# Kernel optimization log

Hardware: AMD Instinct MI355X
Metric: run time of the kernel (lower is better)

Reference implementation:

```python
import jax, jax.numpy as jnp
import numpy as np

B, M, D = 512, 96, 512
H = 8            # num_heads
DH = D // H      # head dim
NC = 3           # num_clusters
BETA = 5
MEM = 1024       # memory_size
EPS = 1e-8


def _l2norm(x, axis=-1):
    # torch F.cosine_similarity clamps each norm at eps=1e-8
    n = jnp.linalg.norm(x, axis=axis, keepdims=True)
    return x / jnp.maximum(n, EPS)


def _dynamic_clustering(sims):
    # sims: (B, M). Sort descending, split into NC equal groups,
    # per-group mean and (unbiased) std. (dynamic_clustering is not
    # defined in the source repo; this is the assumed implementation.)
    s = -jnp.sort(-sims, axis=1)               # descending
    g = s.reshape(B, NC, M // NC)
    means = g.mean(axis=-1)                    # (B, NC)
    stds = jnp.std(g, axis=-1, ddof=1)         # (B, NC)
    return means, stds


def setup_inputs() -> dict:
    key = jax.random.key(0)
    ks = jax.random.split(key, 6)
    vis_global = jax.random.normal(ks[0], (B, D), dtype=jnp.float32)
    text_features = jax.random.normal(ks[1], (B, M, D), dtype=jnp.float32)
    scale = 1.0 / np.sqrt(D)
    in_proj_w = jax.random.normal(ks[2], (3 * D, D), dtype=jnp.float32) * scale
    in_proj_b = jnp.zeros((3 * D,), dtype=jnp.float32)
    out_proj_w = jax.random.normal(ks[3], (D, D), dtype=jnp.float32) * scale
    out_proj_b = jnp.zeros((D,), dtype=jnp.float32)
    text_memory = jax.random.normal(ks[4], (MEM, D), dtype=jnp.float32)
    tau_p_log = jnp.log(jnp.asarray(0.1, dtype=jnp.float32))
    tau_n_log = jnp.log(jnp.asarray(0.05, dtype=jnp.float32))
    return dict(vis_global=vis_global, text_features=text_features,
                in_proj_w=in_proj_w, in_proj_b=in_proj_b,
                out_proj_w=out_proj_w, out_proj_b=out_proj_b,
                text_memory=text_memory, tau_p_log=tau_p_log, tau_n_log=tau_n_log)


def reference(vis_global, text_features, in_proj_w, in_proj_b,
              out_proj_w, out_proj_b, text_memory, tau_p_log, tau_n_log):
    # --- dynamic clustering over visual-text cosine sims ---
    sims = jnp.einsum('bd,bmd->bm', _l2norm(vis_global), _l2norm(text_features))
    means, stds = _dynamic_clustering(sims)
    cluster_scores = means / (stds + 1e-6)     # (B, NC)

    # --- MultiheadAttention: 1-token query, M-token key/value ---
    wq, wk, wv = in_proj_w[:D], in_proj_w[D:2 * D], in_proj_w[2 * D:]
    bq, bk, bv = in_proj_b[:D], in_proj_b[D:2 * D], in_proj_b[2 * D:]
    q = (vis_global @ wq.T + bq).reshape(B, H, DH)              # (B,H,DH)
    k = (text_features @ wk.T + bk).reshape(B, M, H, DH)        # (B,M,H,DH)
    v = (text_features @ wv.T + bv).reshape(B, M, H, DH)
    attn = jax.nn.softmax(jnp.einsum('bhd,bmhd->bhm', q, k) / np.sqrt(DH), axis=-1)
    ctx = jnp.einsum('bhm,bmhd->bhd', attn, v).reshape(B, D)
    corrected = ctx @ out_proj_w.T + out_proj_b                 # (B, D)

    tau_p = jnp.exp(tau_p_log)
    tau_n = jnp.exp(tau_n_log)
    pos_sim = jnp.sum(_l2norm(vis_global) * _l2norm(corrected), axis=-1)  # (B,)

    # memory-bank scatter (ptr starts at 0) + negatives, all detached
    corr_sg = jax.lax.stop_gradient(corrected)
    mem = text_memory.at[0:B].set(corr_sg)
    all_negs = jnp.concatenate([jnp.roll(corr_sg, 1, axis=0), mem], axis=0)  # (B+MEM, D)

    neg_sims = _l2norm(vis_global) @ _l2norm(all_negs).T        # (B, B+MEM)
    hard_negs, _ = jax.lax.top_k(neg_sims, BETA)                # (B, BETA)

    pos_term = jnp.exp(pos_sim / tau_p)
    neg_terms = jnp.exp(hard_negs / tau_n).sum(axis=1)
    loss = -jnp.mean(jnp.log(pos_term / (pos_term + neg_terms + 1e-8)))
    return loss, corrected, cluster_scores
```

## Files before the change

### kernel.cpp

```cpp
#include <hip/hip_runtime.h>
#include <math.h>

typedef unsigned short u16;
typedef unsigned int u32;
typedef __attribute__((ext_vector_type(8))) short short8;
typedef __attribute__((ext_vector_type(4))) float f32x4;

#define EPS 1e-8f

__device__ inline float bf2f(u16 u) {
    union { u32 i; float f; } v; v.i = ((u32)u) << 16; return v.f;
}
__device__ inline u16 f2bf(float f) {
    union { float f; u32 u; } v; v.f = f;
    u32 r = v.u + 0x7fffu + ((v.u >> 16) & 1u);
    return (u16)(r >> 16);
}
__device__ inline u32 pack2(float a, float b) {
    return (u32)f2bf(a) | ((u32)f2bf(b) << 16);
}
__device__ inline float wave_sum(float v) {
    for (int off = 32; off; off >>= 1) v += __shfl_xor(v, off, 64);
    return v;
}

__global__ __launch_bounds__(256) void prep(const float* __restrict__ vis,
                                            const float* __restrict__ ipw,
                                            const float* __restrict__ opw,
                                            float* __restrict__ vis_n,
                                            u16* __restrict__ vis_nb,
                                            u16* __restrict__ vis_b,
                                            u16* __restrict__ wqb,
                                            u16* __restrict__ wvb,
                                            u16* __restrict__ wob,
                                            float* __restrict__ loss0)
{
    int bid = blockIdx.x;
    if (bid >= 128) {
        int i = ((bid - 128) * 256 + threadIdx.x) * 4;
        const float* src; u16* dst; int j;
        if (i < 262144)      { j = i;          src = ipw + j;          dst = wqb + j; }
        else if (i < 524288) { j = i - 262144; src = ipw + 524288 + j; dst = wvb + j; }
        else                 { j = i - 524288; src = opw + j;          dst = wob + j; }
        float4 v = *(const float4*)src;
        uint2 pk; pk.x = pack2(v.x, v.y); pk.y = pack2(v.z, v.w);
        *(uint2*)dst = pk;
        return;
    }
    if (bid == 0 && threadIdx.x == 0) loss0[0] = 0.0f;
    int wave = threadIdx.x >> 6, lane = threadIdx.x & 63;
    int b = bid * 4 + wave;
    const float* row = vis + b * 512 + lane * 8;
    float4 x0 = *(const float4*)row;
    float4 x1 = *(const float4*)(row + 4);
    uint4 rk;
    rk.x = pack2(x0.x, x0.y); rk.y = pack2(x0.z, x0.w);
    rk.z = pack2(x1.x, x1.y); rk.w = pack2(x1.z, x1.w);
    *(uint4*)(vis_b + b*512 + lane*8) = rk;
    float ss = x0.x*x0.x + x0.y*x0.y + x0.z*x0.z + x0.w*x0.w
             + x1.x*x1.x + x1.y*x1.y + x1.z*x1.z + x1.w*x1.w;
    ss = wave_sum(ss);
    float inv = 1.0f / fmaxf(sqrtf(ss), EPS);
    float4 y0, y1;
    y0.x = x0.x*inv; y0.y = x0.y*inv; y0.z = x0.z*inv; y0.w = x0.w*inv;
    y1.x = x1.x*inv; y1.y = x1.y*inv; y1.z = x1.z*inv; y1.w = x1.w*inv;
    *(float4*)(vis_n + b*512 + lane*8)     = y0;
    *(float4*)(vis_n + b*512 + lane*8 + 4) = y1;
    uint4 pk;
    pk.x = pack2(y0.x, y0.y); pk.y = pack2(y0.z, y0.w);
    pk.z = pack2(y1.x, y1.y); pk.w = pack2(y1.z, y1.w);
    *(uint4*)(vis_nb + b*512 + lane*8) = pk;
}

__global__ __launch_bounds__(256) void gemm64(const u16* __restrict__ A, int lda,
                                              const u16* __restrict__ B,
                                              const float* __restrict__ bias,
                                              float* __restrict__ Cf, int ldc)
{
    __shared__ __align__(16) u16 As[64 * 64];
    __shared__ __align__(16) u16 Bs[64 * 64];
    const int t = threadIdx.x, lane = t & 63, w = t >> 6;
    const int m0 = blockIdx.x * 64, n0 = blockIdx.y * 64;
    const int wm = (w >> 1) * 32, wn = (w & 1) * 32;
    const int l16 = lane & 15, quad = lane >> 4;
    const int srow = t >> 3, scol = (t & 7) * 8;

    f32x4 acc[2][2];
    for (int i = 0; i < 2; i++)
        for (int j = 0; j < 2; j++)
            for (int e = 0; e < 4; e++) acc[i][j][e] = 0.f;

    for (int ko = 0; ko < 512; ko += 64) {
        __syncthreads();
        #pragma unroll
        for (int i = 0; i < 2; i++) {
            int row = i * 32 + srow;
            *(uint4*)&As[row * 64 + scol] = *(const uint4*)&A[(size_t)(m0 + row) * lda + ko + scol];
            *(uint4*)&Bs[row * 64 + scol] = *(const uint4*)&B[(size_t)(n0 + row) * 512 + ko + scol];
        }
        __syncthreads();
        #pragma unroll
        for (int ks = 0; ks < 2; ks++) {
            short8 af[2], bfr[2];
            #pragma unroll
            for (int i = 0; i < 2; i++)
                af[i] = *(const short8*)&As[(wm + i * 16 + l16) * 64 + ks * 32 + quad * 8];
            #pragma unroll
            for (int j = 0; j < 2; j++)
                bfr[j] = *(const short8*)&Bs[(wn + j * 16 + l16) * 64 + ks * 32 + quad * 8];
            #pragma unroll
            for (int i = 0; i < 2; i++)
                #pragma unroll
                for (int j = 0; j < 2; j++)
                    acc[i][j] = __builtin_amdgcn_mfma_f32_16x16x32_bf16(af[i], bfr[j], acc[i][j], 0, 0, 0);
        }
    }
    for (int i = 0; i < 2; i++) {
        int row = m0 + wm + i * 16 + quad * 4;
        for (int j = 0; j < 2; j++) {
            int col = n0 + wn + j * 16 + l16;
            float bv = bias ? bias[col] : 0.f;
            for (int r = 0; r < 4; r++)
                Cf[(size_t)(row + r) * ldc + col] = acc[i][j][r] + bv;
        }
    }
}

__global__ __launch_bounds__(256) void gemm_head(const u16* __restrict__ u_allb,
                                                 const u16* __restrict__ wvb,
                                                 const float* __restrict__ bv,
                                                 u16* __restrict__ ctxb)
{
    const int h = blockIdx.y;
    const u16* A = u_allb + h * 512;
    const u16* B = wvb + (size_t)h * 64 * 512;
    __shared__ __align__(16) u16 As[64 * 64];
    __shared__ __align__(16) u16 Bs[64 * 64];
    const int t = threadIdx.x, lane = t & 63, w = t >> 6;
    const int m0 = blockIdx.x * 64;
    const int wm = (w >> 1) * 32, wn = (w & 1) * 32;
    const int l16 = lane & 15, quad = lane >> 4;
    const int srow = t >> 3, scol = (t & 7) * 8;

    f32x4 acc[2][2];
    for (int i = 0; i < 2; i++)
        for (int j = 0; j < 2; j++)
            for (int e = 0; e < 4; e++) acc[i][j][e] = 0.f;

    for (int ko = 0; ko < 512; ko += 64) {
        __syncthreads();
        #pragma unroll
        for (int i = 0; i < 2; i++) {
            int row = i * 32 + srow;
            *(uint4*)&As[row * 64 + scol] = *(const uint4*)&A[(size_t)(m0 + row) * 4096 + ko + scol];
            *(uint4*)&Bs[row * 64 + scol] = *(const uint4*)&B[(size_t)row * 512 + ko + scol];
        }
        __syncthreads();
        #pragma unroll
        for (int ks = 0; ks < 2; ks++) {
            short8 af[2], bfr[2];
            #pragma unroll
            for (int i = 0; i < 2; i++)
                af[i] = *(const short8*)&As[(wm + i * 16 + l16) * 64 + ks * 32 + quad * 8];
            #pragma unroll
            for (int j = 0; j < 2; j++)
                bfr[j] = *(const short8*)&Bs[(wn + j * 16 + l16) * 64 + ks * 32 + quad * 8];
            #pragma unroll
            for (int i = 0; i < 2; i++)
                #pragma unroll
                for (int j = 0; j < 2; j++)
                    acc[i][j] = __builtin_amdgcn_mfma_f32_16x16x32_bf16(af[i], bfr[j], acc[i][j], 0, 0, 0);
        }
    }
    for (int i = 0; i < 2; i++) {
        int row = m0 + wm + i * 16 + quad * 4;
        for (int j = 0; j < 2; j++) {
            int col = wn + j * 16 + l16;
            float bb = bv[h * 64 + col];
            for (int r = 0; r < 4; r++)
                ctxb[(size_t)(row + r) * 512 + h * 64 + col] = f2bf(acc[i][j][r] + bb);
        }
    }
}

__global__ __launch_bounds__(256) void qk_proj(const float* __restrict__ q,
                                               const float* __restrict__ wk,
                                               float* __restrict__ qk_all)
{
    int bg = blockIdx.x, h = blockIdx.y;
    int t = threadIdx.x;
    int j = blockIdx.z * 256 + t;
    __shared__ float q8[8][64];
    {
        int r = t >> 5;
        int d0 = (t & 31) * 2;
        const float* qp = q + (bg * 8 + r) * 512 + h * 64 + d0;
        q8[r][d0] = qp[0]; q8[r][d0 + 1] = qp[1];
    }
    __syncthreads();
    float acc[8] = {0, 0, 0, 0, 0, 0, 0, 0};
    const float* wrow = wk + (size_t)(h * 64) * 512 + j;
    #pragma unroll 4
    for (int d = 0; d < 64; d++) {
        float ww = wrow[(size_t)d * 512];
        #pragma unroll
        for (int r = 0; r < 8; r++) acc[r] += q8[r][d] * ww;
    }
    #pragma unroll
    for (int r = 0; r < 8; r++)
        qk_all[((size_t)(bg * 8 + r) * 8 + h) * 512 + j] = acc[r];
}

__global__ __launch_bounds__(512) void fused_attn(const float* __restrict__ tf,
                                                  const float* __restrict__ vis_n,
                                                  const float* __restrict__ qk_all,
                                                  u16* __restrict__ u_allb,
                                                  float* __restrict__ out_cs)
{
    __shared__ __align__(16) u16 Xs[96 * 520];
    __shared__ __align__(16) u16 Qs[16 * 520];
    __shared__ __align__(16) u16 Ps[16 * 104];
    __shared__ float Sc[16 * 100];
    __shared__ float sm_[96], srt[96], linv[8];

    const int b = blockIdx.x;
    const int t = threadIdx.x, w = t >> 6, lane = t & 63;
    const int l16 = lane & 15, quad = lane >> 4;

    const float4* v4 = (const float4*)(vis_n + b * 512 + lane * 8);
    float4 va = v4[0], vb = v4[1];

    {
        const float4* q4 = (const float4*)(qk_all + ((size_t)b * 8 + w) * 512 + lane * 8);
        float4 a = q4[0], c = q4[1];
        uint4 pk;
        pk.x = pack2(a.x, a.y); pk.y = pack2(a.z, a.w);
        pk.z = pack2(c.x, c.y); pk.w = pack2(c.z, c.w);
        *(uint4*)&Qs[w * 520 + lane * 8] = pk;
    }

    #pragma unroll 2
    for (int i = 0; i < 6; i++) {
        int m0r = w + i * 16;
        int m1r = m0r + 8;
        const float4* x4a = (const float4*)(tf + ((size_t)b * 96 + m0r) * 512 + lane * 8);
        const float4* x4b = (const float4*)(tf + ((size_t)b * 96 + m1r) * 512 + lane * 8);
        float4 a0 = x4a[0], c0 = x4a[1];
        float4 a1 = x4b[0], c1 = x4b[1];
        float ss0 = a0.x*a0.x + a0.y*a0.y + a0.z*a0.z + a0.w*a0.w
                  + c0.x*c0.x + c0.y*c0.y + c0.z*c0.z + c0.w*c0.w;
        float dt0 = a0.x*va.x + a0.y*va.y + a0.z*va.z + a0.w*va.w
                  + c0.x*vb.x + c0.y*vb.y + c0.z*vb.z + c0.w*vb.w;
        float ss1 = a1.x*a1.x + a1.y*a1.y + a1.z*a1.z + a1.w*a1.w
                  + c1.x*c1.x + c1.y*c1.y + c1.z*c1.z + c1.w*c1.w;
        float dt1 = a1.x*va.x + a1.y*va.y + a1.z*va.z + a1.w*va.w
                  + c1.x*vb.x + c1.y*vb.y + c1.z*vb.z + c1.w*vb.w;
        #pragma unroll
        for (int off = 32; off; off >>= 1) {
            ss0 += __shfl_xor(ss0, off, 64);
            dt0 += __shfl_xor(dt0, off, 64);
            ss1 += __shfl_xor(ss1, off, 64);
            dt1 += __shfl_xor(dt1, off, 64);
        }
        if (lane == 0) {
            sm_[m0r] = dt0 / fmaxf(sqrtf(ss0), EPS);
            sm_[m1r] = dt1 / fmaxf(sqrtf(ss1), EPS);
        }
        uint4 pk0, pk1;
        pk0.x = pack2(a0.x, a0.y); pk0.y = pack2(a0.z, a0.w);
        pk0.z = pack2(c0.x, c0.y); pk0.w = pack2(c0.z, c0.w);
        pk1.x = pack2(a1.x, a1.y); pk1.y = pack2(a1.z, a1.w);
        pk1.z = pack2(c1.x, c1.y); pk1.w = pack2(c1.z, c1.w);
        *(uint4*)&Xs[m0r * 520 + lane * 8] = pk0;
        *(uint4*)&Xs[m1r * 520 + lane * 8] = pk1;
    }
    __syncthreads();

    if (w < 6) {
        f32x4 acc;
        for (int e = 0; e < 4; e++) acc[e] = 0.f;
        #pragma unroll
        for (int ks = 0; ks < 16; ks++) {
            short8 a = *(const short8*)&Xs[(w * 16 + l16) * 520 + ks * 32 + quad * 8];
            short8 q = *(const short8*)&Qs[l16 * 520 + ks * 32 + quad * 8];
            acc = __builtin_amdgcn_mfma_f32_16x16x32_bf16(a, q, acc, 0, 0, 0);
        }
        #pragma unroll
        for (int r = 0; r < 4; r++)
            Sc[l16 * 100 + w * 16 + quad * 4 + r] = acc[r] * 0.125f;
    }
    __syncthreads();

    {
        float e0 = __expf(Sc[w * 100 + lane]);
        float e1 = (lane < 32) ? __expf(Sc[w * 100 + 64 + lane]) : 0.f;
        float l = wave_sum(e0 + e1);
        Ps[w * 104 + lane] = f2bf(e0);
        if (lane < 32) Ps[w * 104 + 64 + lane] = f2bf(e1);
        if (lane == 0) linv[w] = 1.0f / l;
    }
    if (t < 96) {
        float v = sm_[t]; int r = 0;
        for (int j = 0; j < 96; j++) {
            float u = sm_[j];
            r += (u > v) || (u == v && j < t);
        }
        srt[r] = v;
    }
    __syncthreads();

    #pragma unroll
    for (int jj = 0; jj < 4; jj++) {
        int n0 = (w * 4 + jj) * 16;
        f32x4 acc;
        for (int e = 0; e < 4; e++) acc[e] = 0.f;
        #pragma unroll
        for (int ks = 0; ks < 3; ks++) {
            short8 ap = *(const short8*)&Ps[l16 * 104 + ks * 32 + quad * 8];
            short8 bx;
            #pragma unroll
            for (int j = 0; j < 8; j++)
                bx[j] = (short)Xs[(ks * 32 + quad * 8 + j) * 520 + n0 + l16];
            acc = __builtin_amdgcn_mfma_f32_16x16x32_bf16(ap, bx, acc, 0, 0, 0);
        }
        if (quad < 2) {
            #pragma unroll
            for (int r = 0; r < 4; r++) {
                int h = quad * 4 + r;
                u_allb[((size_t)b * 8 + h) * 512 + n0 + l16] = f2bf(acc[r] * linv[h]);
            }
        }
    }
    if (t < 3) {
        float mean = 0.f;
        #pragma unroll 8
        for (int i = 0; i < 32; i++) mean += srt[t * 32 + i];
        mean *= (1.0f / 32.0f);
        float var = 0.f;
        #pragma unroll 8
        for (int i = 0; i < 32; i++) { float d = srt[t * 32 + i] - mean; var += d * d; }
        var *= (1.0f / 31.0f);
        out_cs[b * 3 + t] = mean / (sqrtf(var) + 1e-6f);
    }
}

__global__ __launch_bounds__(256) void negs_build(const float* __restrict__ corrected,
                                                  const float* __restrict__ tm,
                                                  const float* __restrict__ vis_n,
                                                  u16* __restrict__ negs_nb,
                                                  float* __restrict__ pos)
{
    int wave = threadIdx.x >> 6, lane = threadIdx.x & 63;
    int j = blockIdx.x * 4 + wave;
    const float* src = (j < 512) ? (corrected + j * 512) : (tm + j * 512);
    const float* row = src + lane * 8;
    float4 x0 = *(const float4*)row;
    float4 x1 = *(const float4*)(row + 4);
    float ss = x0.x*x0.x + x0.y*x0.y + x0.z*x0.z + x0.w*x0.w
             + x1.x*x1.x + x1.y*x1.y + x1.z*x1.z + x1.w*x1.w;
    float dt = 0.f;
    if (j < 512) {
        const float* vn = vis_n + j * 512 + lane * 8;
        float4 v0 = *(const float4*)vn;
        float4 v1 = *(const float4*)(vn + 4);
        dt = x0.x*v0.x + x0.y*v0.y + x0.z*v0.z + x0.w*v0.w
           + x1.x*v1.x + x1.y*v1.y + x1.z*v1.z + x1.w*v1.w;
    }
    ss = wave_sum(ss);
    dt = wave_sum(dt);
    float inv = 1.0f / fmaxf(sqrtf(ss), EPS);
    float4 y0, y1;
    y0.x = x0.x*inv; y0.y = x0.y*inv; y0.z = x0.z*inv; y0.w = x0.w*inv;
    y1.x = x1.x*inv; y1.y = x1.y*inv; y1.z = x1.z*inv; y1.w = x1.w*inv;
    uint4 pk;
    pk.x = pack2(y0.x, y0.y); pk.y = pack2(y0.z, y0.w);
    pk.z = pack2(y1.x, y1.y); pk.w = pack2(y1.z, y1.w);
    *(uint4*)(negs_nb + j * 512 + lane * 8) = pk;
    if (j < 512 && lane == 0) pos[j] = dt * inv;
}

__global__ __launch_bounds__(256) void topk_loss(const float* __restrict__ ns,
                                                 const float* __restrict__ pos,
                                                 const float* __restrict__ tau_p_log,
                                                 const float* __restrict__ tau_n_log,
                                                 float* __restrict__ out_loss)
{
    int b = blockIdx.x, t = threadIdx.x;
    int w = t >> 6, lane = t & 63;
    __shared__ float cand_v[4];
    __shared__ int   cand_m[4];

    const float4 raw = *(const float4*)(ns + b * 1024 + t * 4);
    float lv[4] = {raw.x, raw.y, raw.z, raw.w};
    #pragma unroll
    for (int i = 1; i < 4; i++) {
        float key = lv[i];
        int j = i - 1;
        #pragma unroll
        for (int k = 0; k < 3; k++) {
            if (j >= 0 && lv[j] < key) { lv[j + 1] = lv[j]; j--; }
        }
        lv[j + 1] = key;
    }
    const int mult = (t < 128) ? 2 : 1;
    int lp = 0;

    float tn = expf(tau_n_log[0]);
    float inv_tn = 1.0f / tn;
    float nsum = 0.f;
    int collected = 0;

    for (int round = 0; round < 5 && collected < 5; round++) {
        float head = (lp < 4) ? lv[lp] : -1e30f;
        float mv = head; int ml = lane;
        #pragma unroll
        for (int off = 32; off; off >>= 1) {
            float ov = __shfl_xor(mv, off, 64);
            int   ol = __shfl_xor(ml, off, 64);
            if (ov > mv || (ov == mv && ol < ml)) { mv = ov; ml = ol; }
        }
        if (lane == 0) { cand_v[w] = mv; cand_m[w] = ml; }
        __syncthreads();
        float bv = cand_v[0]; int bw = 0;
        #pragma unroll
        for (int i = 1; i < 4; i++) {
            if (cand_v[i] > bv) { bv = cand_v[i]; bw = i; }
        }
        int bl = cand_m[bw];
        __syncthreads();
        if (w == bw && lane == bl) lp++;
        int wm = ((bw * 64 + bl) < 128) ? 2 : 1;
        int take = (wm < (5 - collected)) ? wm : (5 - collected);
        nsum += (float)take * __expf(bv * inv_tn);
        collected += take;
    }

    if (t == 0) {
        float tp = expf(tau_p_log[0]);
        float p = expf(pos[b] / tp);
        float term = logf(p / (p + nsum + 1e-8f));
        atomicAdd(out_loss, -term * (1.0f / 512.0f));
    }
}

extern "C" void kernel_launch(void* const* d_in, const int* in_sizes, int n_in,
                              void* d_out, int out_size, void* d_ws, size_t ws_size,
                              hipStream_t stream) {
    const float* vis = (const float*)d_in[0];
    const float* tf  = (const float*)d_in[1];
    const float* ipw = (const float*)d_in[2];
    const float* ipb = (const float*)d_in[3];
    const float* opw = (const float*)d_in[4];
    const float* opb = (const float*)d_in[5];
    const float* tm  = (const float*)d_in[6];
    const float* tpl = (const float*)d_in[7];
    const float* tnl = (const float*)d_in[8];

    float* out       = (float*)d_out;
    float* out_loss  = out;
    float* out_corr  = out + 1;
    float* out_cs    = out + 1 + 512 * 512;

    char* p = (char*)d_ws;
    auto alloc = [&](size_t bytes) { char* r = p; p += (bytes + 255) & ~(size_t)255; return r; };
    float* vis_n  = (float*)alloc(512 * 512 * 4);
    u16*   vis_nb = (u16*)  alloc(512 * 512 * 2);
    u16*   vis_b  = (u16*)  alloc(512 * 512 * 2);
    u16*   wqb    = (u16*)  alloc(512 * 512 * 2);
    u16*   wvb    = (u16*)  alloc(512 * 512 * 2);
    u16*   wob    = (u16*)  alloc(512 * 512 * 2);
    float* qws    = (float*)alloc(512 * 512 * 4);
    float* qk_all = (float*)alloc((size_t)512 * 8 * 512 * 4);
    u16*   u_allb = (u16*)  alloc((size_t)512 * 8 * 512 * 2);
    u16*   ctxb   = (u16*)  alloc(512 * 512 * 2);
    u16*   negsb  = (u16*)  alloc(1024 * 512 * 2);
    float* ns     = (float*)alloc(512 * 1024 * 4);
    float* pos    = (float*)alloc(512 * 4);

    const float* wk = ipw + 512 * 512;
    const float* bv = ipb + 2 * 512;

    prep<<<896, 256, 0, stream>>>(vis, ipw, opw, vis_n, vis_nb, vis_b, wqb, wvb, wob, out_loss);
    gemm64<<<dim3(8, 8), 256, 0, stream>>>(vis_b, 512, wqb, ipb, qws, 512);
    qk_proj<<<dim3(64, 8, 2), 256, 0, stream>>>(qws, wk, qk_all);
    fused_attn<<<512, 512, 0, stream>>>(tf, vis_n, qk_all, u_allb, out_cs);
    gemm_head<<<dim3(8, 8), 256, 0, stream>>>(u_allb, wvb, bv, ctxb);
    gemm64<<<dim3(8, 8), 256, 0, stream>>>(ctxb, 512, wob, opb, out_corr, 512);
    negs_build<<<256, 256, 0, stream>>>(out_corr, tm, vis_n, negsb, pos);
    gemm64<<<dim3(8, 16), 256, 0, stream>>>(vis_nb, 512, negsb, nullptr, ns, 1024);
    topk_loss<<<512, 256, 0, stream>>>(ns, pos, tpl, tnl, out_loss);
}
```

Before: 250.5 us.

## Split fused attention into score pass and chunked PV/cluster kernel

Splits the single large fused attention kernel, which uses about 120KB of shared memory and 512 threads per block, into two smaller kernels. The first computes scores and cosine sims over half the tokens per block and writes them to global memory. The second recomputes the softmax and streams text features in 32-row chunks to do the PV MFMA with less shared memory per block. This raises occupancy and parallelism, but reads text_features from HBM twice and adds a launch plus a global round trip for scores. Small cleanups in negs_build and topk_loss are included.

Result: slower. 259.5 us (+3.6%).

```diff
diff --git a/kernel.cpp b/kernel.cpp
--- a/kernel.cpp
+++ b/kernel.cpp
@@ -211,40 +211,40 @@
         qk_all[((size_t)(bg * 8 + r) * 8 + h) * 512 + j] = acc[r];
 }
 
-__global__ __launch_bounds__(512) void fused_attn(const float* __restrict__ tf,
+__global__ __launch_bounds__(256) void score_pass(const float* __restrict__ tf,
                                                   const float* __restrict__ vis_n,
                                                   const float* __restrict__ qk_all,
-                                                  u16* __restrict__ u_allb,
-                                                  float* __restrict__ out_cs)
-{
-    __shared__ __align__(16) u16 Xs[96 * 520];
-    __shared__ __align__(16) u16 Qs[16 * 520];
-    __shared__ __align__(16) u16 Ps[16 * 104];
-    __shared__ float Sc[16 * 100];
-    __shared__ float sm_[96], srt[96], linv[8];
-
-    const int b = blockIdx.x;
+                                                  float* __restrict__ scores,
+                                                  float* __restrict__ sims_g)
+{
+    __shared__ __align__(16) u16 Xs[48 * 520];
+    __shared__ __align__(16) u16 Bs16[16 * 520];
+    const int bid = blockIdx.x;
+    const int b = bid >> 1, half = bid & 1;
     const int t = threadIdx.x, w = t >> 6, lane = t & 63;
     const int l16 = lane & 15, quad = lane >> 4;
 
-    const float4* v4 = (const float4*)(vis_n + b * 512 + lane * 8);
-    float4 va = v4[0], vb = v4[1];
-
-    {
-        const float4* q4 = (const float4*)(qk_all + ((size_t)b * 8 + w) * 512 + lane * 8);
+    #pragma unroll
+    for (int i = 0; i < 2; i++) {
+        int idx = t + 256 * i;
+        int row = idx >> 6, col = (idx & 63) * 8;
+        const float4* q4 = (const float4*)(qk_all + ((size_t)b * 8 + row) * 512 + col);
         float4 a = q4[0], c = q4[1];
         uint4 pk;
         pk.x = pack2(a.x, a.y); pk.y = pack2(a.z, a.w);
         pk.z = pack2(c.x, c.y); pk.w = pack2(c.z, c.w);
-        *(uint4*)&Qs[w * 520 + lane * 8] = pk;
-    }
+        *(uint4*)&Bs16[row * 520 + col] = pk;
+    }
+    const float4* v4 = (const float4*)(vis_n + b * 512 + lane * 8);
+    float4 va = v4[0], vb = v4[1];
 
     #pragma unroll 2
     for (int i = 0; i < 6; i++) {
-        int m0r = w + i * 16;
-        int m1r = m0r + 8;
-        const float4* x4a = (const float4*)(tf + ((size_t)b * 96 + m0r) * 512 + lane * 8);
-        const float4* x4b = (const float4*)(tf + ((size_t)b * 96 + m1r) * 512 + lane * 8);
+        int mA = w * 12 + i, mB = mA + 6;
+        int gA = b * 96 + half * 48 + mA;
+        int gB = b * 96 + half * 48 + mB;
+        const float4* x4a = (const float4*)(tf + (size_t)gA * 512 + lane * 8);
+        const float4* x4b = (const float4*)(tf + (size_t)gB * 512 + lane * 8);
         float4 a0 = x4a[0], c0 = x4a[1];
         float4 a1 = x4b[0], c1 = x4b[1];
         float ss0 = a0.x*a0.x + a0.y*a0.y + a0.z*a0.z + a0.w*a0.w
@@ -263,42 +263,63 @@
             dt1 += __shfl_xor(dt1, off, 64);
         }
         if (lane == 0) {
-            sm_[m0r] = dt0 / fmaxf(sqrtf(ss0), EPS);
-            sm_[m1r] = dt1 / fmaxf(sqrtf(ss1), EPS);
+            sims_g[gA] = dt0 / fmaxf(sqrtf(ss0), EPS);
+            sims_g[gB] = dt1 / fmaxf(sqrtf(ss1), EPS);
         }
         uint4 pk0, pk1;
         pk0.x = pack2(a0.x, a0.y); pk0.y = pack2(a0.z, a0.w);
         pk0.z = pack2(c0.x, c0.y); pk0.w = pack2(c0.z, c0.w);
         pk1.x = pack2(a1.x, a1.y); pk1.y = pack2(a1.z, a1.w);
         pk1.z = pack2(c1.x, c1.y); pk1.w = pack2(c1.z, c1.w);
-        *(uint4*)&Xs[m0r * 520 + lane * 8] = pk0;
-        *(uint4*)&Xs[m1r * 520 + lane * 8] = pk1;
+        *(uint4*)&Xs[mA * 520 + lane * 8] = pk0;
+        *(uint4*)&Xs[mB * 520 + lane * 8] = pk1;
     }
     __syncthreads();
 
-    if (w < 6) {
+    if (w < 3) {
         f32x4 acc;
         for (int e = 0; e < 4; e++) acc[e] = 0.f;
         #pragma unroll
         for (int ks = 0; ks < 16; ks++) {
             short8 a = *(const short8*)&Xs[(w * 16 + l16) * 520 + ks * 32 + quad * 8];
-            short8 q = *(const short8*)&Qs[l16 * 520 + ks * 32 + quad * 8];
+            short8 q = *(const short8*)&Bs16[l16 * 520 + ks * 32 + quad * 8];
             acc = __builtin_amdgcn_mfma_f32_16x16x32_bf16(a, q, acc, 0, 0, 0);
         }
-        #pragma unroll
-        for (int r = 0; r < 4; r++)
-            Sc[l16 * 100 + w * 16 + quad * 4 + r] = acc[r] * 0.125f;
-    }
+        if (l16 < 8) {
+            #pragma unroll
+            for (int r = 0; r < 4; r++) {
+                int m = half * 48 + w * 16 + quad * 4 + r;
+                scores[((size_t)b * 96 + m) * 8 + l16] = acc[r] * 0.125f;
+            }
+        }
+    }
+}
+
+__global__ __launch_bounds__(256) void pv_cluster(const float* __restrict__ tf,
+                                                  const float* __restrict__ scores,
+                                                  const float* __restrict__ sims_g,
+                                                  u16* __restrict__ u_allb,
+                                                  float* __restrict__ out_cs)
+{
+    __shared__ __align__(16) u16 Xs[32 * 520];
+    __shared__ __align__(16) u16 Ps[16 * 104];
+    __shared__ float sm_[96], srt[96], linv[8];
+    const int b = blockIdx.x;
+    const int t = threadIdx.x, w = t >> 6, lane = t & 63;
+    const int l16 = lane & 15, quad = lane >> 4;
+
+    #pragma unroll
+    for (int hh = 0; hh < 2; hh++) {
+        int h = w * 2 + hh;
+        float e0 = __expf(scores[((size_t)b * 96 + lane) * 8 + h]);
+        float e1 = (lane < 32) ? __expf(scores[((size_t)b * 96 + 64 + lane) * 8 + h]) : 0.f;
+        float l = wave_sum(e0 + e1);
+        Ps[h * 104 + lane] = f2bf(e0);
+        if (lane < 32) Ps[h * 104 + 64 + lane] = f2bf(e1);
+        if (lane == 0) linv[h] = 1.0f / l;
+    }
+    if (t < 96) sm_[t] = sims_g[b * 96 + t];
     __syncthreads();
-
-    {
-        float e0 = __expf(Sc[w * 100 + lane]);
-        float e1 = (lane < 32) ? __expf(Sc[w * 100 + 64 + lane]) : 0.f;
-        float l = wave_sum(e0 + e1);
-        Ps[w * 104 + lane] = f2bf(e0);
-        if (lane < 32) Ps[w * 104 + 64 + lane] = f2bf(e1);
-        if (lane == 0) linv[w] = 1.0f / l;
-    }
     if (t < 96) {
         float v = sm_[t]; int r = 0;
         for (int j = 0; j < 96; j++) {
@@ -307,40 +328,57 @@
         }
         srt[r] = v;
     }
-    __syncthreads();
-
+
+    f32x4 acc[8];
     #pragma unroll
-    for (int jj = 0; jj < 4; jj++) {
-        int n0 = (w * 4 + jj) * 16;
-        f32x4 acc;
-        for (int e = 0; e < 4; e++) acc[e] = 0.f;
-        #pragma unroll
-        for (int ks = 0; ks < 3; ks++) {
-            short8 ap = *(const short8*)&Ps[l16 * 104 + ks * 32 + quad * 8];
+    for (int jj = 0; jj < 8; jj++)
+        for (int e = 0; e < 4; e++) acc[jj][e] = 0.f;
+
+    for (int c = 0; c < 3; c++) {
+        #pragma unroll
+        for (int i = 0; i < 8; i++) {
+            int rl = w * 8 + i;
+            const float4* x4 = (const float4*)(tf + ((size_t)b * 96 + c * 32 + rl) * 512 + lane * 8);
+            float4 a = x4[0], cc = x4[1];
+            uint4 pk;
+            pk.x = pack2(a.x, a.y); pk.y = pack2(a.z, a.w);
+            pk.z = pack2(cc.x, cc.y); pk.w = pack2(cc.z, cc.w);
+            *(uint4*)&Xs[rl * 520 + lane * 8] = pk;
+        }
+        __syncthreads();
+        if (c == 0 && t < 3) {
+            float mean = 0.f;
+            #pragma unroll 8
+            for (int i = 0; i < 32; i++) mean += srt[t * 32 + i];
+            mean *= (1.0f / 32.0f);
+            float var = 0.f;
+            #pragma unroll 8
+            for (int i = 0; i < 32; i++) { float d = srt[t * 32 + i] - mean; var += d * d; }
+            var *= (1.0f / 31.0f);
+            out_cs[b * 3 + t] = mean / (sqrtf(var) + 1e-6f);
+        }
+        short8 ap = *(const short8*)&Ps[l16 * 104 + c * 32 + quad * 8];
+        #pragma unroll
+        for (int jj = 0; jj < 8; jj++) {
+            int n0 = (w * 8 + jj) * 16;
             short8 bx;
             #pragma unroll
             for (int j = 0; j < 8; j++)
-                bx[j] = (short)Xs[(ks * 32 + quad * 8 + j) * 520 + n0 + l16];
-            acc = __builtin_amdgcn_mfma_f32_16x16x32_bf16(ap, bx, acc, 0, 0, 0);
-        }
-        if (quad < 2) {
+                bx[j] = (short)Xs[(quad * 8 + j) * 520 + n0 + l16];
+            acc[jj] = __builtin_amdgcn_mfma_f32_16x16x32_bf16(ap, bx, acc[jj], 0, 0, 0);
+        }
+        if (c < 2) __syncthreads();
+    }
+    if (quad < 2) {
+        #pragma unroll
+        for (int jj = 0; jj < 8; jj++) {
+            int n0 = (w * 8 + jj) * 16;
             #pragma unroll
             for (int r = 0; r < 4; r++) {
                 int h = quad * 4 + r;
-                u_allb[((size_t)b * 8 + h) * 512 + n0 + l16] = f2bf(acc[r] * linv[h]);
+                u_allb[((size_t)b * 8 + h) * 512 + n0 + l16] = f2bf(acc[jj][r] * linv[h]);
             }
         }
-    }
-    if (t < 3) {
-        float mean = 0.f;
-        #pragma unroll 8
-        for (int i = 0; i < 32; i++) mean += srt[t * 32 + i];
-        mean *= (1.0f / 32.0f);
-        float var = 0.f;
-        #pragma unroll 8
-        for (int i = 0; i < 32; i++) { float d = srt[t * 32 + i] - mean; var += d * d; }
-        var *= (1.0f / 31.0f);
-        out_cs[b * 3 + t] = mean / (sqrtf(var) + 1e-6f);
     }
 }
 
@@ -369,13 +407,10 @@
     ss = wave_sum(ss);
     dt = wave_sum(dt);
     float inv = 1.0f / fmaxf(sqrtf(ss), EPS);
-    float4 y0, y1;
-    y0.x = x0.x*inv; y0.y = x0.y*inv; y0.z = x0.z*inv; y0.w = x0.w*inv;
-    y1.x = x1.x*inv; y1.y = x1.y*inv; y1.z = x1.z*inv; y1.w = x1.w*inv;
     uint4 pk;
-    pk.x = pack2(y0.x, y0.y); pk.y = pack2(y0.z, y0.w);
-    pk.z = pack2(y1.x, y1.y); pk.w = pack2(y1.z, y1.w);
-    *(uint4*)(negs_nb + j * 512 + lane * 8) = pk;
+    pk.x = pack2(x0.x*inv, x0.y*inv); pk.y = pack2(x0.z*inv, x0.w*inv);
+    pk.z = pack2(x1.x*inv, x1.y*inv); pk.w = pack2(x1.z*inv, x1.w*inv);
+    *(uint4*)(negs_nb + (size_t)j * 512 + lane * 8) = pk;
     if (j < 512 && lane == 0) pos[j] = dt * inv;
 }
 
@@ -402,7 +437,6 @@
         }
         lv[j + 1] = key;
     }
-    const int mult = (t < 128) ? 2 : 1;
     int lp = 0;
 
     float tn = expf(tau_n_log[0]);
@@ -471,6 +505,8 @@
     u16*   wob    = (u16*)  alloc(512 * 512 * 2);
     float* qws    = (float*)alloc(512 * 512 * 4);
     float* qk_all = (float*)alloc((size_t)512 * 8 * 512 * 4);
+    float* scores = (float*)alloc((size_t)512 * 96 * 8 * 4);
+    float* sims_g = (float*)alloc(512 * 96 * 4);
     u16*   u_allb = (u16*)  alloc((size_t)512 * 8 * 512 * 2);
     u16*   ctxb   = (u16*)  alloc(512 * 512 * 2);
     u16*   negsb  = (u16*)  alloc(1024 * 512 * 2);
@@ -483,7 +519,8 @@
     prep<<<896, 256, 0, stream>>>(vis, ipw, opw, vis_n, vis_nb, vis_b, wqb, wvb, wob, out_loss);
     gemm64<<<dim3(8, 8), 256, 0, stream>>>(vis_b, 512, wqb, ipb, qws, 512);
     qk_proj<<<dim3(64, 8, 2), 256, 0, stream>>>(qws, wk, qk_all);
-    fused_attn<<<512, 512, 0, stream>>>(tf, vis_n, qk_all, u_allb, out_cs);
+    score_pass<<<1024, 256, 0, stream>>>(tf, vis_n, qk_all, scores, sims_g);
+    pv_cluster<<<512, 256, 0, stream>>>(tf, scores, sims_g, u_allb, out_cs);
     gemm_head<<<dim3(8, 8), 256, 0, stream>>>(u_allb, wvb, bv, ctxb);
     gemm64<<<dim3(8, 8), 256, 0, stream>>>(ctxb, 512, wob, opb, out_corr, 512);
     negs_build<<<256, 256, 0, stream>>>(out_corr, tm, vis_n, negsb, pos);
```
